# Optimization experiments

Hardware: AMD Instinct MI355X
Metric: run time of the kernel (lower is better)

## Reference

```python
import jax, jax.numpy as jnp
import numpy as np

KERNEL = 16
STRIDE = 4


def setup_inputs() -> dict:
    key = jax.random.key(0)
    k1, k2 = jax.random.split(key)
    N, L = 1024, 8192
    inp = jax.random.normal(k1, (N, L), dtype=jnp.float32)
    # nn.init.uniform_(And_weight, 0.3, 0.7)
    And_weight = jax.random.uniform(k2, (1, KERNEL), dtype=jnp.float32, minval=0.3, maxval=0.7)
    return {"input": inp, "And_weight": And_weight}


def reference(input, And_weight):
    N, L = input.shape
    k = And_weight.shape[1]
    starts = jnp.arange(0, L - k + 1, STRIDE)           # [W]
    idx = starts[:, None] + jnp.arange(k)[None, :]       # [W, k]
    windows = input[:, idx]                              # [N, W, k] strided sliding windows
    rho = windows * And_weight[0][None, None, :]         # weighted robustness
    # Temporal_Operators.Always == min over the temporal window (STL 'Always')
    return jnp.min(rho, axis=-1)                         # [N, W]
```

## Files before the change

kernel.cpp:

```cpp
#include <hip/hip_runtime.h>


#define KER 16
#define STR 4
#define ROWLEN 8192
#define NWIN 2045

__global__ __launch_bounds__(256) void and_conv_kernel(
    const float* __restrict__ inp,
    const float* __restrict__ wgt,
    float* __restrict__ out) {
    const int w = blockIdx.x * 256 + threadIdx.x;
    const int n = blockIdx.y;
    if (w >= NWIN) return;

    const float4* row = (const float4*)(inp + (size_t)n * ROWLEN);
    float4 c0 = row[w];
    float4 c1 = row[w + 1];
    float4 c2 = row[w + 2];
    float4 c3 = row[w + 3];

    const float4* wv = (const float4*)wgt;
    float4 w0 = wv[0];
    float4 w1 = wv[1];
    float4 w2 = wv[2];
    float4 w3 = wv[3];

    float m0 = fminf(fminf(c0.x * w0.x, c0.y * w0.y),
                     fminf(c0.z * w0.z, c0.w * w0.w));
    float m1 = fminf(fminf(c1.x * w1.x, c1.y * w1.y),
                     fminf(c1.z * w1.z, c1.w * w1.w));
    float m2 = fminf(fminf(c2.x * w2.x, c2.y * w2.y),
                     fminf(c2.z * w2.z, c2.w * w2.w));
    float m3 = fminf(fminf(c3.x * w3.x, c3.y * w3.y),
                     fminf(c3.z * w3.z, c3.w * w3.w));

    out[(size_t)n * NWIN + w] = fminf(fminf(m0, m1), fminf(m2, m3));
}

extern "C" void kernel_launch(void* const* d_in, const int* in_sizes, int n_in,
                              void* d_out, int out_size, void* d_ws, size_t ws_size,
                              hipStream_t stream) {
    const float* inp = (const float*)d_in[0];
    const float* wgt = (const float*)d_in[1];
    float* out = (float*)d_out;

    const int N = in_sizes[0] / ROWLEN;
    dim3 grid((NWIN + 255) / 256, N);
    and_conv_kernel<<<grid, dim3(256), 0, stream>>>(inp, wgt, out);
}
```

Before: 75.35 us.

## Stage full input row in shared memory, one block per row

```diff
diff --git a/kernel.cpp b/kernel.cpp
--- a/kernel.cpp
+++ b/kernel.cpp
@@ -4,38 +4,59 @@
 #define KER 16
 #define STR 4
 #define ROWLEN 8192
+#define NCHUNK (ROWLEN / 4)
 #define NWIN 2045
+#define BLOCK 256
+#define PER_T (NCHUNK / BLOCK)
 
-__global__ __launch_bounds__(256) void and_conv_kernel(
+__global__ __launch_bounds__(BLOCK) void and_conv_kernel(
     const float* __restrict__ inp,
     const float* __restrict__ wgt,
     float* __restrict__ out) {
-    const int w = blockIdx.x * 256 + threadIdx.x;
-    const int n = blockIdx.y;
-    if (w >= NWIN) return;
+    __shared__ float4 srow[NCHUNK];
 
-    const float4* row = (const float4*)(inp + (size_t)n * ROWLEN);
-    float4 c0 = row[w];
-    float4 c1 = row[w + 1];
-    float4 c2 = row[w + 2];
-    float4 c3 = row[w + 3];
+    const int t = threadIdx.x;
+    const int n = blockIdx.x;
+
+    const float4* __restrict__ row = (const float4*)(inp + (size_t)n * ROWLEN);
+
+#pragma unroll
+    for (int j = 0; j < PER_T; ++j) {
+        const int c = t + BLOCK * j;
+        srow[c] = row[c];
+    }
 
     const float4* wv = (const float4*)wgt;
-    float4 w0 = wv[0];
-    float4 w1 = wv[1];
-    float4 w2 = wv[2];
-    float4 w3 = wv[3];
+    const float4 w0 = wv[0];
+    const float4 w1 = wv[1];
+    const float4 w2 = wv[2];
+    const float4 w3 = wv[3];
 
-    float m0 = fminf(fminf(c0.x * w0.x, c0.y * w0.y),
-                     fminf(c0.z * w0.z, c0.w * w0.w));
-    float m1 = fminf(fminf(c1.x * w1.x, c1.y * w1.y),
-                     fminf(c1.z * w1.z, c1.w * w1.w));
-    float m2 = fminf(fminf(c2.x * w2.x, c2.y * w2.y),
-                     fminf(c2.z * w2.z, c2.w * w2.w));
-    float m3 = fminf(fminf(c3.x * w3.x, c3.y * w3.y),
-                     fminf(c3.z * w3.z, c3.w * w3.w));
+    __syncthreads();
 
-    out[(size_t)n * NWIN + w] = fminf(fminf(m0, m1), fminf(m2, m3));
+    float* __restrict__ orow = out + (size_t)n * NWIN;
+
+#pragma unroll
+    for (int j = 0; j < PER_T; ++j) {
+        const int w = t + BLOCK * j;
+        if (w < NWIN) {
+            const float4 c0 = srow[w];
+            const float4 c1 = srow[w + 1];
+            const float4 c2 = srow[w + 2];
+            const float4 c3 = srow[w + 3];
+
+            const float m0 = fminf(fminf(c0.x * w0.x, c0.y * w0.y),
+                                   fminf(c0.z * w0.z, c0.w * w0.w));
+            const float m1 = fminf(fminf(c1.x * w1.x, c1.y * w1.y),
+                                   fminf(c1.z * w1.z, c1.w * w1.w));
+            const float m2 = fminf(fminf(c2.x * w2.x, c2.y * w2.y),
+                                   fminf(c2.z * w2.z, c2.w * w2.w));
+            const float m3 = fminf(fminf(c3.x * w3.x, c3.y * w3.y),
+                                   fminf(c3.z * w3.z, c3.w * w3.w));
+
+            orow[w] = fminf(fminf(m0, m1), fminf(m2, m3));
+        }
+    }
 }
 
 extern "C" void kernel_launch(void* const* d_in, const int* in_sizes, int n_in,
@@ -46,6 +67,5 @@
     float* out = (float*)d_out;
 
     const int N = in_sizes[0] / ROWLEN;
-    dim3 grid((NWIN + 255) / 256, N);
-    and_conv_kernel<<<grid, dim3(256), 0, stream>>>(inp, wgt, out);
+    and_conv_kernel<<<dim3(N), dim3(BLOCK), 0, stream>>>(inp, wgt, out);
 }
```

New measurement: 75.60 us. About the same (+0.3%).
